# Kernel tuning notes

Measured on AMD Instinct MI355X. Metric: run time of the kernel, lower is better.

## Reference

```python
import jax, jax.numpy as jnp
import numpy as np

N, E = 50000, 800000
C, H = 64, 128  # out_channels, 2*out_channels


def gcn_conv(x, src, dst, W, b):
    # PyG GCNConv: h = x @ W; add self loops; sym-normalized sum aggregation; + bias
    n = x.shape[0]
    h = x @ W
    deg = jnp.zeros((n,), h.dtype).at[dst].add(1.0) + 1.0  # in-degree + self loop
    dinv = jax.lax.rsqrt(deg)
    norm = dinv[src] * dinv[dst]                            # [E]
    agg = jnp.zeros_like(h).at[dst].add(h[src] * norm[:, None])
    agg = agg + h * (1.0 / deg)[:, None]                    # self-loop term
    return agg + b


def setup_inputs() -> dict:
    key = jax.random.key(0)
    ks = jax.random.split(key, 12)
    g = lambda k, shp: (jax.random.normal(k, shp, jnp.float32) * 0.05)
    return {
        "x": jax.random.randint(ks[0], (N, 1), 0, 28),
        "edge_index": jax.random.randint(ks[1], (2, E), 0, N),
        "emb_W": g(ks[2], (28, H)),
        "W1": g(ks[3], (H, H)), "b1": jnp.zeros((H,), jnp.float32),
        "W2": g(ks[4], (H, H)), "b2": jnp.zeros((H,), jnp.float32),
        "W3": g(ks[5], (H, C)), "b3": jnp.zeros((C,), jnp.float32),
        "Wmu": g(ks[6], (C, C)), "bmu": jnp.zeros((C,), jnp.float32),
        "Wls": g(ks[7], (C, C)), "bls": jnp.zeros((C,), jnp.float32),
    }


def reference(x, edge_index, emb_W, W1, b1, W2, b2, W3, b3, Wmu, bmu, Wls, bls):
    src, dst = edge_index[0], edge_index[1]
    h = emb_W[x[:, 0]]                                      # [N, H] molecular embedding
    # PyG GCN(num_layers=3): ReLU between layers, none after last
    h = jax.nn.relu(gcn_conv(h, src, dst, W1, b1))
    h = jax.nn.relu(gcn_conv(h, src, dst, W2, b2))
    h = gcn_conv(h, src, dst, W3, b3)
    h = jax.nn.relu(h)                                      # .relu() in encoder forward
    mu = gcn_conv(h, src, dst, Wmu, bmu)
    logstd = gcn_conv(h, src, dst, Wls, bls)
    return (mu, logstd)
```

## Files before the change

### kernel.cpp

```cpp
#include <hip/hip_runtime.h>
#include <hip/hip_bf16.h>
#include <cstddef>



__global__ __launch_bounds__(256) void k_hist(const int* __restrict__ dst,
                                              int* __restrict__ hist_g, int e) {
    __shared__ int h[256];
    const int tid = threadIdx.x;
    h[tid] = 0;
    __syncthreads();
    const int e0 = blockIdx.x * 4096;
    const int e1 = min(e0 + 4096, e);
    for (int j = e0 + tid; j < e1; j += 256) atomicAdd(&h[dst[j] >> 8], 1);
    __syncthreads();
    hist_g[blockIdx.x * 256 + tid] = h[tid];
}

__global__ __launch_bounds__(256) void k_scanT(const int* __restrict__ hist_g,
                                               int* __restrict__ tbase,
                                               int* __restrict__ bsum, int ntile) {
    const int b = blockIdx.x;
    const int t = threadIdx.x;
    const int lane = t & 63, wv = t >> 6;
    __shared__ int wsum[4];
    int carry = 0;
    for (int c = 0; c < ntile; c += 256) {
        int tt = c + t;
        int v0 = (tt < ntile) ? hist_g[tt * 256 + b] : 0;
        int v = v0;
#pragma unroll
        for (int d = 1; d < 64; d <<= 1) {
            int w = __shfl_up(v, d, 64);
            if (lane >= d) v += w;
        }
        if (lane == 63) wsum[wv] = v;
        __syncthreads();
        int woff = 0;
        for (int w = 0; w < wv; ++w) woff += wsum[w];
        int tot = wsum[0] + wsum[1] + wsum[2] + wsum[3];
        if (tt < ntile) tbase[tt * 256 + b] = carry + woff + v - v0;
        carry += tot;
        __syncthreads();
    }
    if (t == 0) bsum[b] = carry;
}

__global__ __launch_bounds__(256) void k_bscan2(const int* __restrict__ bsum,
                                                int* __restrict__ boff) {
    __shared__ int wsum[4];
    const int t = threadIdx.x;
    const int lane = t & 63, wv = t >> 6;
    int v0 = bsum[t];
    int v = v0;
#pragma unroll
    for (int d = 1; d < 64; d <<= 1) {
        int w = __shfl_up(v, d, 64);
        if (lane >= d) v += w;
    }
    if (lane == 63) wsum[wv] = v;
    __syncthreads();
    int woff = 0;
    for (int w = 0; w < wv; ++w) woff += wsum[w];
    int excl = woff + v - v0;
    boff[t] = excl;
    if (t == 255) boff[256] = excl + v0;
}

__global__ __launch_bounds__(256) void k_binA3(const int* __restrict__ src,
                                               const int* __restrict__ dst,
                                               const int* __restrict__ boff,
                                               const int* __restrict__ tbase,
                                               int* __restrict__ packed, int e) {
    __shared__ int hist[256];
    __shared__ int base[256];
    const int tid = threadIdx.x;
    const int e0 = blockIdx.x * 4096;
    const int e1 = min(e0 + 4096, e);
    hist[tid] = 0;
    base[tid] = boff[tid] + tbase[blockIdx.x * 256 + tid];
    __syncthreads();
    for (int j = e0 + tid; j < e1; j += 256) {
        int d = dst[j];
        int b = d >> 8;
        int r = atomicAdd(&hist[b], 1);
        packed[base[b] + r] = ((d & 255) << 16) | src[j];
    }
}

#define BCAP 6144
__global__ __launch_bounds__(1024) void k_binB2(const int* __restrict__ packed,
                                                const int* __restrict__ boff,
                                                const int* __restrict__ x,
                                                int* __restrict__ rptr,
                                                float* __restrict__ dinv,
                                                int2* __restrict__ xd,
                                                int* __restrict__ col,
                                                int n) {
    __shared__ int hist[256];
    __shared__ int cur[256];
    __shared__ int wsum[4];
    __shared__ int buf[BCAP];
    const int tid = threadIdx.x;
    const int node0 = blockIdx.x << 8;
    const int node1 = min(node0 + 256, n);
    const int ebeg = boff[blockIdx.x];
    const int eend = boff[blockIdx.x + 1];
    const int cnt = eend - ebeg;

    if (tid < 256) hist[tid] = 0;
    __syncthreads();
    for (int j = tid; j < cnt; j += 1024) atomicAdd(&hist[packed[ebeg + j] >> 16], 1);
    __syncthreads();

    int deg = 0, v = 0;
    if (tid < 256) {
        const int lane = tid & 63, wv = tid >> 6;
        deg = hist[tid];
        v = deg;
#pragma unroll
        for (int d = 1; d < 64; d <<= 1) {
            int w = __shfl_up(v, d, 64);
            if (lane >= d) v += w;
        }
        if (lane == 63) wsum[wv] = v;
    }
    __syncthreads();
    if (tid < 256) {
        const int wv = tid >> 6;
        int woff = 0;
        for (int w = 0; w < wv; ++w) woff += wsum[w];
        const int excl = woff + v - deg;
        cur[tid] = excl;
        const int node = node0 + tid;
        if (node < node1) {
            rptr[node] = ebeg + excl;
            float dv = 1.0f / sqrtf((float)(deg + 1));
            dinv[node] = dv;
            xd[node] = make_int2(x[node], __float_as_int(dv));
        }
        if (node1 == n && tid == 0) rptr[n] = eend;
    }
    __syncthreads();

    if (cnt <= BCAP) {
        for (int j = tid; j < cnt; j += 1024) {
            int p = packed[ebeg + j];
            int pos = atomicAdd(&cur[p >> 16], 1);
            buf[pos] = p & 0xffff;
        }
        __syncthreads();
        for (int j = tid; j < cnt; j += 1024) col[ebeg + j] = buf[j];
    } else {
        for (int j = tid; j < cnt; j += 1024) {
            int p = packed[ebeg + j];
            int pos = atomicAdd(&cur[p >> 16], 1);
            col[ebeg + pos] = p & 0xffff;
        }
    }
}

__global__ __launch_bounds__(256) void k_prepW(const float* __restrict__ embW,
                                               const float* __restrict__ W1,
                                               const float* __restrict__ Wmu,
                                               const float* __restrict__ Wls,
                                               float* __restrict__ M,
                                               float* __restrict__ Wcat,
                                               int V, int nsm) {
    if ((int)blockIdx.x < nsm) {
        const int r = blockIdx.x * 2 + (threadIdx.x >> 7);
        const int c = threadIdx.x & 127;
        if (r >= V) return;
        float a0 = 0.f, a1 = 0.f;
        const float* er = embW + (size_t)r * 128;
#pragma unroll 4
        for (int k = 0; k < 128; k += 2) {
            a0 = fmaf(er[k], W1[(size_t)k * 128 + c], a0);
            a1 = fmaf(er[k + 1], W1[(size_t)(k + 1) * 128 + c], a1);
        }
        M[(size_t)r * 128 + c] = a0 + a1;
    } else {
        int i = (blockIdx.x - nsm) * 256 + threadIdx.x;
        if (i < 64 * 128) {
            int k = i >> 7, c = i & 127;
            Wcat[i] = (c < 64) ? Wmu[k * 64 + c] : Wls[k * 64 + (c - 64)];
        }
    }
}

__global__ __launch_bounds__(256) void k_gather_l1(const float* __restrict__ M,
                                                   const int* __restrict__ rptr,
                                                   const int* __restrict__ col,
                                                   const int2* __restrict__ xd,
                                                   const float* __restrict__ b,
                                                   float* __restrict__ out,
                                                   int n, int V) {
    __shared__ float sh[32 * 128];
    for (int f = threadIdx.x; f < V * 32; f += 256)
        ((float4*)sh)[f] = ((const float4*)M)[f];
    __syncthreads();

    const int wave = threadIdx.x >> 6;
    const int lane = threadIdx.x & 63;
    const int node = blockIdx.x * 4 + wave;
    if (node >= n) return;
    const int beg = rptr[node], end = rptr[node + 1];
    int j = beg;

    float ax0 = 0.f, ay0 = 0.f, ax1 = 0.f, ay1 = 0.f;
    const int lo = 2 * lane;
    if (end - beg >= 8) {
        int s[8];
#pragma unroll
        for (int u = 0; u < 8; ++u) s[u] = col[j + u];
        j += 8;
        while (true) {
            int2 p[8];
#pragma unroll
            for (int u = 0; u < 8; ++u) p[u] = xd[s[u]];
            const bool more = (j + 8 <= end);
            int sn[8];
            if (more) {
#pragma unroll
                for (int u = 0; u < 8; ++u) sn[u] = col[j + u];
            }
#pragma unroll
            for (int u = 0; u < 8; ++u) {
                float dv = __int_as_float(p[u].y);
                float2 v = *(const float2*)&sh[p[u].x * 128 + lo];
                if (u & 1) { ax1 = fmaf(dv, v.x, ax1); ay1 = fmaf(dv, v.y, ay1); }
                else       { ax0 = fmaf(dv, v.x, ax0); ay0 = fmaf(dv, v.y, ay0); }
            }
            if (!more) break;
#pragma unroll
            for (int u = 0; u < 8; ++u) s[u] = sn[u];
            j += 8;
        }
    }
    for (; j < end; ++j) {
        int2 p = xd[col[j]];
        float dv = __int_as_float(p.y);
        float2 v = *(const float2*)&sh[p.x * 128 + lo];
        ax0 = fmaf(dv, v.x, ax0); ay0 = fmaf(dv, v.y, ay0);
    }
    int2 pn = xd[node];
    float dn = __int_as_float(pn.y);
    float2 sv = *(const float2*)&sh[pn.x * 128 + lo];
    float2 bb = ((const float2*)b)[lane];
    float ox = (ax0 + ax1 + dn * sv.x) * dn + bb.x;
    float oy = (ay0 + ay1 + dn * sv.y) * dn + bb.y;
    ((float2*)out)[(size_t)node * 64 + lane] = {ox, oy};
}

template <int K, int COUT, bool RELU>
__global__ __launch_bounds__(256) void k_matmul(const float* __restrict__ in,
                                                const float* __restrict__ W,
                                                const float* __restrict__ dinv,
                                                float* __restrict__ out, int n) {
    constexpr int BM = 128, KC = 32, LDI = KC + 4;
    constexpr int CT = COUT / 16;
    __shared__ float sIn[BM * LDI];
    __shared__ float sW[KC * COUT];

    const int tid = threadIdx.x;
    const int row0 = blockIdx.x * BM;
    const int tc = tid & 15;
    const int tr = tid >> 4;

    float acc[8][CT];
#pragma unroll
    for (int j = 0; j < 8; ++j)
#pragma unroll
        for (int c = 0; c < CT; ++c) acc[j][c] = 0.f;

    const int sr = tid >> 3;
    const int sk = (tid & 7) * 4;

    float4 pf[4];
#pragma unroll
    for (int p = 0; p < 4; ++p) {
        int gr = row0 + p * 32 + sr;
        pf[p] = (gr < n) ? *(const float4*)&in[(size_t)gr * K + sk]
                         : float4{0.f, 0.f, 0.f, 0.f};
    }

    for (int kc = 0; kc < K; kc += KC) {
#pragma unroll
        for (int p = 0; p < 4; ++p) {
            float4 v = pf[p];
            if (RELU) {
                v.x = fmaxf(v.x, 0.f); v.y = fmaxf(v.y, 0.f);
                v.z = fmaxf(v.z, 0.f); v.w = fmaxf(v.w, 0.f);
            }
            *(float4*)&sIn[(p * 32 + sr) * LDI + sk] = v;
        }
        for (int f4 = tid; f4 < KC * COUT / 4; f4 += 256)
            *(float4*)&sW[f4 * 4] = *(const float4*)&W[(size_t)kc * COUT + f4 * 4];
        __syncthreads();

        if (kc + KC < K) {
#pragma unroll
            for (int p = 0; p < 4; ++p) {
                int gr = row0 + p * 32 + sr;
                pf[p] = (gr < n) ? *(const float4*)&in[(size_t)gr * K + kc + KC + sk]
                                 : float4{0.f, 0.f, 0.f, 0.f};
            }
        }

        for (int kk = 0; kk < KC; kk += 4) {
            float4 a[8];
#pragma unroll
            for (int j = 0; j < 8; ++j)
                a[j] = *(const float4*)&sIn[(tr * 8 + j) * LDI + kk];
#pragma unroll
            for (int t = 0; t < 4; ++t) {
                float4 w0 = *(const float4*)&sW[(kk + t) * COUT + tc * 4];
                float4 w1;
                if constexpr (CT == 8)
                    w1 = *(const float4*)&sW[(kk + t) * COUT + COUT / 2 + tc * 4];
#pragma unroll
                for (int j = 0; j < 8; ++j) {
                    float av = (t == 0) ? a[j].x : (t == 1) ? a[j].y
                             : (t == 2) ? a[j].z : a[j].w;
                    acc[j][0] = fmaf(av, w0.x, acc[j][0]);
                    acc[j][1] = fmaf(av, w0.y, acc[j][1]);
                    acc[j][2] = fmaf(av, w0.z, acc[j][2]);
                    acc[j][3] = fmaf(av, w0.w, acc[j][3]);
                    if constexpr (CT == 8) {
                        acc[j][4] = fmaf(av, w1.x, acc[j][4]);
                        acc[j][5] = fmaf(av, w1.y, acc[j][5]);
                        acc[j][6] = fmaf(av, w1.z, acc[j][6]);
                        acc[j][7] = fmaf(av, w1.w, acc[j][7]);
                    }
                }
            }
        }
        __syncthreads();
    }

#pragma unroll
    for (int j = 0; j < 8; ++j) {
        int gr = row0 + tr * 8 + j;
        if (gr < n) {
            float dv = dinv[gr];
            float4 o0 = {acc[j][0] * dv, acc[j][1] * dv, acc[j][2] * dv, acc[j][3] * dv};
            *(float4*)&out[(size_t)gr * COUT + tc * 4] = o0;
            if constexpr (CT == 8) {
                float4 o1 = {acc[j][4] * dv, acc[j][5] * dv, acc[j][6] * dv, acc[j][7] * dv};
                *(float4*)&out[(size_t)gr * COUT + COUT / 2 + tc * 4] = o1;
            }
        }
    }
}

__global__ __launch_bounds__(256) void k_mm_heads(const float* __restrict__ in,
                                                  const float* __restrict__ W,
                                                  const float* __restrict__ bmu,
                                                  const float* __restrict__ bls,
                                                  float* __restrict__ mu,
                                                  float* __restrict__ ls, int n) {
    constexpr int BM = 128, KC = 32, LDI = KC + 4, K = 64, COUT = 128;
    __shared__ float sIn[BM * LDI];
    __shared__ float sW[KC * COUT];

    const int tid = threadIdx.x;
    const int row0 = blockIdx.x * BM;
    const int tc = tid & 15;
    const int tr = tid >> 4;

    float acc[8][8];
#pragma unroll
    for (int j = 0; j < 8; ++j)
#pragma unroll
        for (int c = 0; c < 8; ++c) acc[j][c] = 0.f;

    const int sr = tid >> 3;
    const int sk = (tid & 7) * 4;

    float4 pf[4];
#pragma unroll
    for (int p = 0; p < 4; ++p) {
        int gr = row0 + p * 32 + sr;
        pf[p] = (gr < n) ? *(const float4*)&in[(size_t)gr * K + sk]
                         : float4{0.f, 0.f, 0.f, 0.f};
    }

    for (int kc = 0; kc < K; kc += KC) {
#pragma unroll
        for (int p = 0; p < 4; ++p)
            *(float4*)&sIn[(p * 32 + sr) * LDI + sk] = pf[p];
        for (int f4 = tid; f4 < KC * COUT / 4; f4 += 256)
            *(float4*)&sW[f4 * 4] = *(const float4*)&W[(size_t)kc * COUT + f4 * 4];
        __syncthreads();

        if (kc + KC < K) {
#pragma unroll
            for (int p = 0; p < 4; ++p) {
                int gr = row0 + p * 32 + sr;
                pf[p] = (gr < n) ? *(const float4*)&in[(size_t)gr * K + kc + KC + sk]
                                 : float4{0.f, 0.f, 0.f, 0.f};
            }
        }

        for (int kk = 0; kk < KC; kk += 4) {
            float4 a[8];
#pragma unroll
            for (int j = 0; j < 8; ++j)
                a[j] = *(const float4*)&sIn[(tr * 8 + j) * LDI + kk];
#pragma unroll
            for (int t = 0; t < 4; ++t) {
                float4 w0 = *(const float4*)&sW[(kk + t) * COUT + tc * 4];
                float4 w1 = *(const float4*)&sW[(kk + t) * COUT + 64 + tc * 4];
#pragma unroll
                for (int j = 0; j < 8; ++j) {
                    float av = (t == 0) ? a[j].x : (t == 1) ? a[j].y
                             : (t == 2) ? a[j].z : a[j].w;
                    acc[j][0] = fmaf(av, w0.x, acc[j][0]);
                    acc[j][1] = fmaf(av, w0.y, acc[j][1]);
                    acc[j][2] = fmaf(av, w0.z, acc[j][2]);
                    acc[j][3] = fmaf(av, w0.w, acc[j][3]);
                    acc[j][4] = fmaf(av, w1.x, acc[j][4]);
                    acc[j][5] = fmaf(av, w1.y, acc[j][5]);
                    acc[j][6] = fmaf(av, w1.z, acc[j][6]);
                    acc[j][7] = fmaf(av, w1.w, acc[j][7]);
                }
            }
        }
        __syncthreads();
    }

    float4 bm = ((const float4*)bmu)[tc];
    float4 bl = ((const float4*)bls)[tc];
#pragma unroll
    for (int j = 0; j < 8; ++j) {
        int gr = row0 + tr * 8 + j;
        if (gr < n) {
            float4 o0 = {acc[j][0] + bm.x, acc[j][1] + bm.y, acc[j][2] + bm.z, acc[j][3] + bm.w};
            float4 o1 = {acc[j][4] + bl.x, acc[j][5] + bl.y, acc[j][6] + bl.z, acc[j][7] + bl.w};
            *(float4*)&mu[(size_t)gr * 64 + tc * 4] = o0;
            *(float4*)&ls[(size_t)gr * 64 + tc * 4] = o1;
        }
    }
}

__global__ __launch_bounds__(256) void k_gather128p(const float* __restrict__ tab,
                                                    const int* __restrict__ rptr,
                                                    const int* __restrict__ col,
                                                    const float* __restrict__ dinv,
                                                    const float* __restrict__ b,
                                                    float* __restrict__ out, int n) {
    const int wave = threadIdx.x >> 6;
    const int lane = threadIdx.x & 63;
    const int g = lane >> 5;
    const int q = lane & 31;
    const int node = blockIdx.x * 4 + wave;
    if (node >= n) return;
    const int beg = rptr[node], end = rptr[node + 1];

    float4 acc = {0.f, 0.f, 0.f, 0.f};
    int j = beg;
    if (j < end) {
        int s[8]; bool val[8];
#pragma unroll
        for (int u = 0; u < 8; ++u) {
            int ei = j + 2 * u + g;
            val[u] = ei < end;
            s[u] = val[u] ? col[ei] : node;
        }
        j += 16;
        while (true) {
            float4 v[8];
#pragma unroll
            for (int u = 0; u < 8; ++u)
                v[u] = *(const float4*)&tab[(size_t)s[u] * 128 + q * 4];
            const bool more = j < end;
            int sn[8]; bool vn[8];
            if (more) {
#pragma unroll
                for (int u = 0; u < 8; ++u) {
                    int ei = j + 2 * u + g;
                    vn[u] = ei < end;
                    sn[u] = vn[u] ? col[ei] : node;
                }
            }
#pragma unroll
            for (int u = 0; u < 8; ++u) {
                if (val[u]) {
                    acc.x += v[u].x; acc.y += v[u].y;
                    acc.z += v[u].z; acc.w += v[u].w;
                }
            }
            if (!more) break;
#pragma unroll
            for (int u = 0; u < 8; ++u) { s[u] = sn[u]; val[u] = vn[u]; }
            j += 16;
        }
    }
    acc.x += __shfl_xor(acc.x, 32, 64); acc.y += __shfl_xor(acc.y, 32, 64);
    acc.z += __shfl_xor(acc.z, 32, 64); acc.w += __shfl_xor(acc.w, 32, 64);

    if (g == 0) {
        float4 self = *(const float4*)&tab[(size_t)node * 128 + q * 4];
        float dn = dinv[node];
        float4 bb = ((const float4*)b)[q];
        float4 o = {(acc.x + self.x) * dn + bb.x, (acc.y + self.y) * dn + bb.y,
                    (acc.z + self.z) * dn + bb.z, (acc.w + self.w) * dn + bb.w};
        *(float4*)&out[(size_t)node * 128 + q * 4] = o;
    }
}

template <int MODE>
__global__ __launch_bounds__(256) void k_gather64p(const float* __restrict__ tab,
                                                   const int* __restrict__ rptr,
                                                   const int* __restrict__ col,
                                                   const float* __restrict__ dinv,
                                                   const float* __restrict__ b,
                                                   float* __restrict__ out, int n) {
    const int wave = threadIdx.x >> 6;
    const int lane = threadIdx.x & 63;
    const int g = lane >> 4;
    const int q = lane & 15;
    const int node = blockIdx.x * 4 + wave;
    if (node >= n) return;
    const int beg = rptr[node], end = rptr[node + 1];

    float4 acc = {0.f, 0.f, 0.f, 0.f};
    int j = beg;
    if (j < end) {
        int s[4]; bool val[4];
#pragma unroll
        for (int u = 0; u < 4; ++u) {
            int ei = j + 4 * u + g;
            val[u] = ei < end;
            s[u] = val[u] ? col[ei] : node;
        }
        j += 16;
        while (true) {
            float4 v[4];
#pragma unroll
            for (int u = 0; u < 4; ++u)
                v[u] = *(const float4*)&tab[(size_t)s[u] * 64 + q * 4];
            const bool more = j < end;
            int sn[4]; bool vn[4];
            if (more) {
#pragma unroll
                for (int u = 0; u < 4; ++u) {
                    int ei = j + 4 * u + g;
                    vn[u] = ei < end;
                    sn[u] = vn[u] ? col[ei] : node;
                }
            }
#pragma unroll
            for (int u = 0; u < 4; ++u) {
                if (val[u]) {
                    acc.x += v[u].x; acc.y += v[u].y;
                    acc.z += v[u].z; acc.w += v[u].w;
                }
            }
            if (!more) break;
#pragma unroll
            for (int u = 0; u < 4; ++u) { s[u] = sn[u]; val[u] = vn[u]; }
            j += 16;
        }
    }
    acc.x += __shfl_xor(acc.x, 16, 64); acc.y += __shfl_xor(acc.y, 16, 64);
    acc.z += __shfl_xor(acc.z, 16, 64); acc.w += __shfl_xor(acc.w, 16, 64);
    acc.x += __shfl_xor(acc.x, 32, 64); acc.y += __shfl_xor(acc.y, 32, 64);
    acc.z += __shfl_xor(acc.z, 32, 64); acc.w += __shfl_xor(acc.w, 32, 64);

    if (g == 0) {
        float4 self = *(const float4*)&tab[(size_t)node * 64 + q * 4];
        float dn = dinv[node];
        float4 o = {(acc.x + self.x) * dn, (acc.y + self.y) * dn,
                    (acc.z + self.z) * dn, (acc.w + self.w) * dn};
        if constexpr (MODE == 1) {
            float4 bb = ((const float4*)b)[q];
            o.x = fmaxf(o.x + bb.x, 0.f) * dn;
            o.y = fmaxf(o.y + bb.y, 0.f) * dn;
            o.z = fmaxf(o.z + bb.z, 0.f) * dn;
            o.w = fmaxf(o.w + bb.w, 0.f) * dn;
        }
        *(float4*)&out[(size_t)node * 64 + q * 4] = o;
    }
}

extern "C" void kernel_launch(void* const* d_in, const int* in_sizes, int n_in,
                              void* d_out, int out_size, void* d_ws, size_t ws_size,
                              hipStream_t stream) {
    const int*   x    = (const int*)d_in[0];
    const int*   ei   = (const int*)d_in[1];
    const float* embW = (const float*)d_in[2];
    const float* W1   = (const float*)d_in[3];
    const float* b1   = (const float*)d_in[4];
    const float* W2   = (const float*)d_in[5];
    const float* b2   = (const float*)d_in[6];
    const float* W3   = (const float*)d_in[7];
    const float* b3   = (const float*)d_in[8];
    const float* Wmu  = (const float*)d_in[9];
    const float* bmu  = (const float*)d_in[10];
    const float* Wls  = (const float*)d_in[11];
    const float* bls  = (const float*)d_in[12];

    const int n = in_sizes[0];
    const int e = in_sizes[1] / 2;
    const int V = in_sizes[2] / 128;
    const int* src = ei;
    const int* dst = ei + e;

    char* w = (char*)d_ws;
    auto alloc = [&](size_t bytes) {
        char* p = w;
        w += (bytes + 255) & ~(size_t)255;
        return p;
    };
    float* bufA = (float*)alloc((size_t)n * 128 * 4);
    float* bufB = (float*)alloc((size_t)n * 128 * 4);
    float* hW   = (float*)alloc((size_t)n * 128 * 4);
    int*   rptr = (int*)alloc((size_t)(n + 1) * 4);
    int*   col  = (int*)alloc((size_t)e * 4);
    int*   pck  = (int*)alloc((size_t)e * 4);
    float* dinv = (float*)alloc((size_t)n * 4);
    int2*  xd   = (int2*)alloc((size_t)n * 8);
    float* Wcat = (float*)alloc((size_t)64 * 128 * 4);
    float* Msm  = (float*)alloc((size_t)32 * 128 * 4);
    int*   boff = (int*)alloc((size_t)257 * 4);
    int*   bsum = (int*)alloc((size_t)256 * 4);

    const int ntile = (e + 4095) / 4096;
    const int nbuck = (n + 255) / 256;
    int* hist_g = (int*)alloc((size_t)ntile * 256 * 4);
    int* tbase  = (int*)alloc((size_t)ntile * 256 * 4);

    const int nsm = (V + 1) / 2;

    k_hist  <<<ntile, 256, 0, stream>>>(dst, hist_g, e);
    k_scanT <<<256, 256, 0, stream>>>(hist_g, tbase, bsum, ntile);
    k_bscan2<<<1, 256, 0, stream>>>(bsum, boff);
    k_binA3 <<<ntile, 256, 0, stream>>>(src, dst, boff, tbase, pck, e);
    k_binB2 <<<nbuck, 1024, 0, stream>>>(pck, boff, x, rptr, dinv, xd, col, n);
    k_prepW <<<nsm + 32, 256, 0, stream>>>(embW, W1, Wmu, Wls, Msm, Wcat, V, nsm);

    const int gmm = (n + 127) / 128;
    const int ggt = (n + 3) / 4;
    float* mu = (float*)d_out;
    float* ls = (float*)d_out + (size_t)n * 64;

    k_gather_l1<<<ggt, 256, 0, stream>>>(Msm, rptr, col, xd, b1, bufA, n, V);
    k_matmul<128, 128, true><<<gmm, 256, 0, stream>>>(bufA, W2, dinv, hW, n);
    k_gather128p<<<ggt, 256, 0, stream>>>(hW, rptr, col, dinv, b2, bufB, n);
    k_matmul<128, 64, true><<<gmm, 256, 0, stream>>>(bufB, W3, dinv, hW, n);
    k_gather64p<1><<<ggt, 256, 0, stream>>>(hW, rptr, col, dinv, b3, bufA, n);
    k_gather64p<2><<<ggt, 256, 0, stream>>>(bufA, rptr, col, dinv, bmu, bufB, n);
    k_mm_heads<<<gmm, 256, 0, stream>>>(bufB, Wcat, bmu, bls, mu, ls, n);
}
```

Before: 262.0 us.

## Merge weight prep into histogram launch, persist layer-1 gather, use nontemporal stores

Folds the weight-preparation kernel into the histogram kernel as extra blocks, which removes one launch from the chain. Turns the layer-1 gather into a grid-stride loop over a fixed 2048 blocks, so the shared-memory copy of the embedding table is loaded once per block instead of once per 4 nodes. Switches the gather output stores to nontemporal stores so their results are less likely to stay in cache. The nontemporal hint may hurt when the next kernel immediately reads those outputs.

```diff
diff --git a/kernel.cpp b/kernel.cpp
--- a/kernel.cpp
+++ b/kernel.cpp
@@ -3,18 +3,49 @@
 #include <cstddef>
 
 
-
-__global__ __launch_bounds__(256) void k_hist(const int* __restrict__ dst,
-                                              int* __restrict__ hist_g, int e) {
-    __shared__ int h[256];
+typedef float v4f __attribute__((ext_vector_type(4)));
+typedef float v2f __attribute__((ext_vector_type(2)));
+
+
+__global__ __launch_bounds__(256) void k_histprep(const int* __restrict__ dst,
+                                                  int* __restrict__ hist_g, int e,
+                                                  int ntile,
+                                                  const float* __restrict__ embW,
+                                                  const float* __restrict__ W1,
+                                                  const float* __restrict__ Wmu,
+                                                  const float* __restrict__ Wls,
+                                                  float* __restrict__ M,
+                                                  float* __restrict__ Wcat,
+                                                  int V, int nsm) {
     const int tid = threadIdx.x;
-    h[tid] = 0;
-    __syncthreads();
-    const int e0 = blockIdx.x * 4096;
-    const int e1 = min(e0 + 4096, e);
-    for (int j = e0 + tid; j < e1; j += 256) atomicAdd(&h[dst[j] >> 8], 1);
-    __syncthreads();
-    hist_g[blockIdx.x * 256 + tid] = h[tid];
+    if ((int)blockIdx.x < ntile) {
+        __shared__ int h[256];
+        h[tid] = 0;
+        __syncthreads();
+        const int e0 = blockIdx.x * 4096;
+        const int e1 = min(e0 + 4096, e);
+        for (int j = e0 + tid; j < e1; j += 256) atomicAdd(&h[dst[j] >> 8], 1);
+        __syncthreads();
+        hist_g[blockIdx.x * 256 + tid] = h[tid];
+    } else if ((int)blockIdx.x < ntile + nsm) {
+        const int r = (blockIdx.x - ntile) * 2 + (tid >> 7);
+        const int c = tid & 127;
+        if (r >= V) return;
+        float a0 = 0.f, a1 = 0.f;
+        const float* er = embW + (size_t)r * 128;
+#pragma unroll 4
+        for (int k = 0; k < 128; k += 2) {
+            a0 = fmaf(er[k], W1[(size_t)k * 128 + c], a0);
+            a1 = fmaf(er[k + 1], W1[(size_t)(k + 1) * 128 + c], a1);
+        }
+        M[(size_t)r * 128 + c] = a0 + a1;
+    } else {
+        int i = (blockIdx.x - ntile - nsm) * 256 + tid;
+        if (i < 64 * 128) {
+            int k = i >> 7, c = i & 127;
+            Wcat[i] = (c < 64) ? Wmu[k * 64 + c] : Wls[k * 64 + (c - 64)];
+        }
+    }
 }
 
 __global__ __launch_bounds__(256) void k_scanT(const int* __restrict__ hist_g,
@@ -160,34 +191,6 @@
     }
 }
 
-__global__ __launch_bounds__(256) void k_prepW(const float* __restrict__ embW,
-                                               const float* __restrict__ W1,
-                                               const float* __restrict__ Wmu,
-                                               const float* __restrict__ Wls,
-                                               float* __restrict__ M,
-                                               float* __restrict__ Wcat,
-                                               int V, int nsm) {
-    if ((int)blockIdx.x < nsm) {
-        const int r = blockIdx.x * 2 + (threadIdx.x >> 7);
-        const int c = threadIdx.x & 127;
-        if (r >= V) return;
-        float a0 = 0.f, a1 = 0.f;
-        const float* er = embW + (size_t)r * 128;
-#pragma unroll 4
-        for (int k = 0; k < 128; k += 2) {
-            a0 = fmaf(er[k], W1[(size_t)k * 128 + c], a0);
-            a1 = fmaf(er[k + 1], W1[(size_t)(k + 1) * 128 + c], a1);
-        }
-        M[(size_t)r * 128 + c] = a0 + a1;
-    } else {
-        int i = (blockIdx.x - nsm) * 256 + threadIdx.x;
-        if (i < 64 * 128) {
-            int k = i >> 7, c = i & 127;
-            Wcat[i] = (c < 64) ? Wmu[k * 64 + c] : Wls[k * 64 + (c - 64)];
-        }
-    }
-}
-
 __global__ __launch_bounds__(256) void k_gather_l1(const float* __restrict__ M,
                                                    const int* __restrict__ rptr,
                                                    const int* __restrict__ col,
@@ -202,54 +205,55 @@
 
     const int wave = threadIdx.x >> 6;
     const int lane = threadIdx.x & 63;
-    const int node = blockIdx.x * 4 + wave;
-    if (node >= n) return;
-    const int beg = rptr[node], end = rptr[node + 1];
-    int j = beg;
-
-    float ax0 = 0.f, ay0 = 0.f, ax1 = 0.f, ay1 = 0.f;
     const int lo = 2 * lane;
-    if (end - beg >= 8) {
-        int s[8];
-#pragma unroll
-        for (int u = 0; u < 8; ++u) s[u] = col[j + u];
-        j += 8;
-        while (true) {
-            int2 p[8];
-#pragma unroll
-            for (int u = 0; u < 8; ++u) p[u] = xd[s[u]];
-            const bool more = (j + 8 <= end);
-            int sn[8];
-            if (more) {
-#pragma unroll
-                for (int u = 0; u < 8; ++u) sn[u] = col[j + u];
-            }
-#pragma unroll
-            for (int u = 0; u < 8; ++u) {
-                float dv = __int_as_float(p[u].y);
-                float2 v = *(const float2*)&sh[p[u].x * 128 + lo];
-                if (u & 1) { ax1 = fmaf(dv, v.x, ax1); ay1 = fmaf(dv, v.y, ay1); }
-                else       { ax0 = fmaf(dv, v.x, ax0); ay0 = fmaf(dv, v.y, ay0); }
-            }
-            if (!more) break;
-#pragma unroll
-            for (int u = 0; u < 8; ++u) s[u] = sn[u];
+    const int stride = gridDim.x * 4;
+
+    for (int node = blockIdx.x * 4 + wave; node < n; node += stride) {
+        const int beg = rptr[node], end = rptr[node + 1];
+        int j = beg;
+        float ax0 = 0.f, ay0 = 0.f, ax1 = 0.f, ay1 = 0.f;
+        if (end - beg >= 8) {
+            int s[8];
+#pragma unroll
+            for (int u = 0; u < 8; ++u) s[u] = col[j + u];
             j += 8;
-        }
-    }
-    for (; j < end; ++j) {
-        int2 p = xd[col[j]];
-        float dv = __int_as_float(p.y);
-        float2 v = *(const float2*)&sh[p.x * 128 + lo];
-        ax0 = fmaf(dv, v.x, ax0); ay0 = fmaf(dv, v.y, ay0);
-    }
-    int2 pn = xd[node];
-    float dn = __int_as_float(pn.y);
-    float2 sv = *(const float2*)&sh[pn.x * 128 + lo];
-    float2 bb = ((const float2*)b)[lane];
-    float ox = (ax0 + ax1 + dn * sv.x) * dn + bb.x;
-    float oy = (ay0 + ay1 + dn * sv.y) * dn + bb.y;
-    ((float2*)out)[(size_t)node * 64 + lane] = {ox, oy};
+            while (true) {
+                int2 p[8];
+#pragma unroll
+                for (int u = 0; u < 8; ++u) p[u] = xd[s[u]];
+                const bool more = (j + 8 <= end);
+                int sn[8];
+                if (more) {
+#pragma unroll
+                    for (int u = 0; u < 8; ++u) sn[u] = col[j + u];
+                }
+#pragma unroll
+                for (int u = 0; u < 8; ++u) {
+                    float dv = __int_as_float(p[u].y);
+                    float2 vv = *(const float2*)&sh[p[u].x * 128 + lo];
+                    if (u & 1) { ax1 = fmaf(dv, vv.x, ax1); ay1 = fmaf(dv, vv.y, ay1); }
+                    else       { ax0 = fmaf(dv, vv.x, ax0); ay0 = fmaf(dv, vv.y, ay0); }
+                }
+                if (!more) break;
+#pragma unroll
+                for (int u = 0; u < 8; ++u) s[u] = sn[u];
+                j += 8;
+            }
+        }
+        for (; j < end; ++j) {
+            int2 p = xd[col[j]];
+            float dv = __int_as_float(p.y);
+            float2 vv = *(const float2*)&sh[p.x * 128 + lo];
+            ax0 = fmaf(dv, vv.x, ax0); ay0 = fmaf(dv, vv.y, ay0);
+        }
+        int2 pn = xd[node];
+        float dn = __int_as_float(pn.y);
+        float2 sv = *(const float2*)&sh[pn.x * 128 + lo];
+        float2 bb = ((const float2*)b)[lane];
+        v2f o = {(ax0 + ax1 + dn * sv.x) * dn + bb.x,
+                 (ay0 + ay1 + dn * sv.y) * dn + bb.y};
+        __builtin_nontemporal_store(o, (v2f*)out + (size_t)node * 64 + lane);
+    }
 }
 
 template <int K, int COUT, bool RELU>
@@ -503,9 +507,9 @@
         float4 self = *(const float4*)&tab[(size_t)node * 128 + q * 4];
         float dn = dinv[node];
         float4 bb = ((const float4*)b)[q];
-        float4 o = {(acc.x + self.x) * dn + bb.x, (acc.y + self.y) * dn + bb.y,
-                    (acc.z + self.z) * dn + bb.z, (acc.w + self.w) * dn + bb.w};
-        *(float4*)&out[(size_t)node * 128 + q * 4] = o;
+        v4f o = {(acc.x + self.x) * dn + bb.x, (acc.y + self.y) * dn + bb.y,
+                 (acc.z + self.z) * dn + bb.z, (acc.w + self.w) * dn + bb.w};
+        __builtin_nontemporal_store(o, (v4f*)&out[(size_t)node * 128 + q * 4]);
     }
 }
 
@@ -571,8 +575,8 @@
     if (g == 0) {
         float4 self = *(const float4*)&tab[(size_t)node * 64 + q * 4];
         float dn = dinv[node];
-        float4 o = {(acc.x + self.x) * dn, (acc.y + self.y) * dn,
-                    (acc.z + self.z) * dn, (acc.w + self.w) * dn};
+        v4f o = {(acc.x + self.x) * dn, (acc.y + self.y) * dn,
+                 (acc.z + self.z) * dn, (acc.w + self.w) * dn};
         if constexpr (MODE == 1) {
             float4 bb = ((const float4*)b)[q];
             o.x = fmaxf(o.x + bb.x, 0.f) * dn;
@@ -580,7 +584,7 @@
             o.z = fmaxf(o.z + bb.z, 0.f) * dn;
             o.w = fmaxf(o.w + bb.w, 0.f) * dn;
         }
-        *(float4*)&out[(size_t)node * 64 + q * 4] = o;
+        __builtin_nontemporal_store(o, (v4f*)&out[(size_t)node * 64 + q * 4]);
     }
 }
 
@@ -633,19 +637,20 @@
 
     const int nsm = (V + 1) / 2;
 
-    k_hist  <<<ntile, 256, 0, stream>>>(dst, hist_g, e);
+    k_histprep<<<ntile + nsm + 32, 256, 0, stream>>>(dst, hist_g, e, ntile,
+                                                     embW, W1, Wmu, Wls,
+                                                     Msm, Wcat, V, nsm);
     k_scanT <<<256, 256, 0, stream>>>(hist_g, tbase, bsum, ntile);
     k_bscan2<<<1, 256, 0, stream>>>(bsum, boff);
     k_binA3 <<<ntile, 256, 0, stream>>>(src, dst, boff, tbase, pck, e);
     k_binB2 <<<nbuck, 1024, 0, stream>>>(pck, boff, x, rptr, dinv, xd, col, n);
-    k_prepW <<<nsm + 32, 256, 0, stream>>>(embW, W1, Wmu, Wls, Msm, Wcat, V, nsm);
 
     const int gmm = (n + 127) / 128;
     const int ggt = (n + 3) / 4;
     float* mu = (float*)d_out;
     float* ls = (float*)d_out + (size_t)n * 64;
 
-    k_gather_l1<<<ggt, 256, 0, stream>>>(Msm, rptr, col, xd, b1, bufA, n, V);
+    k_gather_l1<<<2048, 256, 0, stream>>>(Msm, rptr, col, xd, b1, bufA, n, V);
     k_matmul<128, 128, true><<<gmm, 256, 0, stream>>>(bufA, W2, dinv, hW, n);
     k_gather128p<<<ggt, 256, 0, stream>>>(hW, rptr, col, dinv, b2, bufB, n);
     k_matmul<128, 64, true><<<gmm, 256, 0, stream>>>(bufB, W3, dinv, hW, n);
```

Result: faster. 248.4 us (-5.2%).
